# Performance work log

Hardware: AMD Instinct MI355X
Metric: run time of the kernel (lower is better)

## Reference

```python
import jax, jax.numpy as jnp
import numpy as np

N_EMBD = 1024
HEAD_SIZE = 64
T = 8192
LN_EPS = 1e-5


def _layer_norm(x, gamma, beta):
    mu = jnp.mean(x, axis=-1, keepdims=True)
    var = jnp.mean(jnp.square(x - mu), axis=-1, keepdims=True)
    return (x - mu) * jax.lax.rsqrt(var + LN_EPS) * gamma + beta


def setup_inputs() -> dict:
    key = jax.random.key(0)
    ks = jax.random.split(key, 10)
    s_in = 1.0 / np.sqrt(N_EMBD)
    s_hs = 1.0 / np.sqrt(HEAD_SIZE)
    s_ff = 1.0 / np.sqrt(4 * N_EMBD)
    return {
        "x": jax.random.normal(ks[0], (T, N_EMBD), dtype=jnp.float32),
        "Wk": jax.random.uniform(ks[1], (N_EMBD, HEAD_SIZE), jnp.float32, -s_in, s_in),
        "Wq": jax.random.uniform(ks[2], (N_EMBD, HEAD_SIZE), jnp.float32, -s_in, s_in),
        "Wv": jax.random.uniform(ks[3], (N_EMBD, HEAD_SIZE), jnp.float32, -s_in, s_in),
        "Wp": jax.random.uniform(ks[4], (HEAD_SIZE, N_EMBD), jnp.float32, -s_hs, s_hs),
        "W1": jax.random.uniform(ks[5], (N_EMBD, 4 * N_EMBD), jnp.float32, -s_in, s_in),
        "b1": jax.random.uniform(ks[6], (4 * N_EMBD,), jnp.float32, -s_in, s_in),
        "W2": jax.random.uniform(ks[7], (4 * N_EMBD, N_EMBD), jnp.float32, -s_ff, s_ff),
        "b2": jax.random.uniform(ks[8], (N_EMBD,), jnp.float32, -s_ff, s_ff),
        "g1": jnp.ones((N_EMBD,), jnp.float32),
        "be1": jnp.zeros((N_EMBD,), jnp.float32),
        "g2": jnp.ones((N_EMBD,), jnp.float32),
        "be2": jnp.zeros((N_EMBD,), jnp.float32),
    }


def reference(x, Wk, Wq, Wv, Wp, W1, b1, W2, b2, g1, be1, g2, be2):
    Tn = x.shape[0]
    k = x @ Wk            # (T, hs)
    q = x @ Wq            # (T, hs)
    v = x @ Wv            # (T, hs)
    wei = (q @ k.T) * (HEAD_SIZE ** -0.5)       # (T, T)
    causal = jnp.tril(jnp.ones((Tn, Tn), dtype=bool))
    wei = jnp.where(causal, wei, -jnp.inf)
    wei = jax.nn.softmax(wei, axis=-1)
    attn = (wei @ v) @ Wp                        # (T, n_embd)
    x1 = _layer_norm(x + attn, g1, be1)
    y = jax.nn.relu(x1 @ W1 + b1) @ W2 + b2      # FFN
    return _layer_norm(x1 + y, g2, be2)
```

## Files before the change

kernel.cpp:

```cpp
#include <hip/hip_runtime.h>
#include <hip/hip_bf16.h>

#define T_SEQ 8192
#define NE 1024
#define FF 4096

typedef __bf16 bf16_t;
typedef __bf16 bf16x8 __attribute__((ext_vector_type(8)));
typedef __bf16 bf16x4 __attribute__((ext_vector_type(4)));
typedef float f32x4 __attribute__((ext_vector_type(4)));

__device__ __forceinline__ void gll16(const void* g, void* l) {
    __builtin_amdgcn_global_load_lds(
        (const __attribute__((address_space(1))) void*)g,
        (__attribute__((address_space(3))) void*)l, 16, 0, 0);
}

__global__ __launch_bounds__(256) void cast_f32_bf16(const float* __restrict__ in,
                                                     bf16_t* __restrict__ out, int n4) {
    int i = blockIdx.x * 256 + threadIdx.x;
    if (i >= n4) return;
    float4 v = ((const float4*)in)[i];
    bf16x4 h;
    h[0] = (bf16_t)v.x; h[1] = (bf16_t)v.y; h[2] = (bf16_t)v.z; h[3] = (bf16_t)v.w;
    ((bf16x4*)out)[i] = h;
}

__global__ __launch_bounds__(256) void build_wkqv(const float* __restrict__ Wk,
                                                  const float* __restrict__ Wq,
                                                  const float* __restrict__ Wv,
                                                  bf16_t* __restrict__ out) {
    int idx = blockIdx.x * 256 + threadIdx.x;
    int n  = idx >> 10;
    int kk = idx & 1023;
    float v = 0.f;
    if (n < 64)       v = Wk[kk * 64 + n];
    else if (n < 128) v = Wq[kk * 64 + (n - 64)] * 0.125f;
    else if (n < 192) v = Wv[kk * 64 + (n - 128)];
    out[idx] = (bf16_t)v;
}

__global__ __launch_bounds__(256) void tcast(const float* __restrict__ in,
                                             bf16_t* __restrict__ out, int R, int C) {
    __shared__ bf16_t tl[64][66];
    const int bc = blockIdx.x << 6, br = blockIdx.y << 6;
    const int tx = threadIdx.x & 63, ty = threadIdx.x >> 6;
#pragma unroll
    for (int j = 0; j < 16; ++j) {
        const int r = ty + j * 4;
        tl[r][tx] = (bf16_t)in[(size_t)(br + r) * C + bc + tx];
    }
    __syncthreads();
#pragma unroll
    for (int j = 0; j < 16; ++j) {
        const int r = ty + j * 4;
        out[(size_t)(bc + r) * R + br + tx] = tl[tx][r];
    }
}

template <int EPI>
__global__ __launch_bounds__(256, 2)
void gemm_bt(const bf16_t* __restrict__ A, const bf16_t* __restrict__ Bt,
             int M, int N, int K,
             float* __restrict__ outf,
             bf16_t* __restrict__ ob0, bf16_t* __restrict__ ob1, bf16_t* __restrict__ ob2,
             const float* __restrict__ res, const float* __restrict__ bias) {
    const int tid  = threadIdx.x;
    const int lane = tid & 63;
    const int tiles_n = N >> 7;
    const int tm = blockIdx.x / tiles_n;
    const int tn = blockIdx.x % tiles_n;
    const int brow = tm << 7, bcol = tn << 7;

    __shared__ __align__(16) bf16_t As[128 * 32];
    __shared__ __align__(16) bf16_t Bs[128 * 32];

    const int c1 = tid, c2 = tid + 256;
    const int s1 = (((c1 & 3) ^ ((c1 >> 3) & 3)) * 8);
    const int s2 = (((c2 & 3) ^ ((c2 >> 3) & 3)) * 8);
    const bf16_t* gA1 = A + (size_t)(brow + (c1 >> 2)) * K + s1;
    const bf16_t* gA2 = A + (size_t)(brow + (c2 >> 2)) * K + s2;
    const bf16_t* gB1 = Bt + (size_t)(bcol + (c1 >> 2)) * K + s1;
    const bf16_t* gB2 = Bt + (size_t)(bcol + (c2 >> 2)) * K + s2;
    bf16_t* lA1 = As + c1 * 8; bf16_t* lA2 = As + c2 * 8;
    bf16_t* lB1 = Bs + c1 * 8; bf16_t* lB2 = Bs + c2 * 8;

    const int wv = tid >> 6;
    const int wr = (wv >> 1) * 64, wc = (wv & 1) * 64;
    const int arow  = wr + (lane & 15);
    const int brf   = wc + (lane & 15);
    const int koff = (((lane >> 4) ^ ((lane >> 1) & 3)) * 8);

    f32x4 acc[4][4];
#pragma unroll
    for (int i = 0; i < 4; ++i)
#pragma unroll
        for (int j = 0; j < 4; ++j) acc[i][j] = (f32x4){0.f, 0.f, 0.f, 0.f};

    for (int k0 = 0; k0 < K; k0 += 32) {
        gll16(gA1, lA1); gll16(gA2, lA2);
        gll16(gB1, lB1); gll16(gB2, lB2);
        gA1 += 32; gA2 += 32; gB1 += 32; gB2 += 32;
        __syncthreads();
        bf16x8 af[4], bfr[4];
#pragma unroll
        for (int mi = 0; mi < 4; ++mi)
            af[mi] = *(const bf16x8*)(As + (arow + mi * 16) * 32 + koff);
#pragma unroll
        for (int ni = 0; ni < 4; ++ni)
            bfr[ni] = *(const bf16x8*)(Bs + (brf + ni * 16) * 32 + koff);
#pragma unroll
        for (int mi = 0; mi < 4; ++mi)
#pragma unroll
            for (int ni = 0; ni < 4; ++ni)
                acc[mi][ni] = __builtin_amdgcn_mfma_f32_16x16x32_bf16(
                    af[mi], bfr[ni], acc[mi][ni], 0, 0, 0);
        __syncthreads();
    }

    const int r0 = brow + wr + ((lane >> 4) << 2);
    const int c0 = bcol + wc + (lane & 15);
#pragma unroll
    for (int mi = 0; mi < 4; ++mi)
#pragma unroll
        for (int ni = 0; ni < 4; ++ni)
#pragma unroll
            for (int r = 0; r < 4; ++r) {
                const int row = r0 + mi * 16 + r;
                const int col = c0 + ni * 16;
                const float v = acc[mi][ni][r];
                if constexpr (EPI == 0) {
                    if (col < 64)       ob0[row * 64 + col] = (bf16_t)v;
                    else if (col < 128) ob1[row * 64 + (col - 64)] = (bf16_t)v;
                    else if (col < 192) ob2[(size_t)(col - 128) * T_SEQ + row] = (bf16_t)v;
                } else if constexpr (EPI == 1) {
                    outf[(size_t)row * N + col] = res[(size_t)row * N + col] + v;
                } else if constexpr (EPI == 2) {
                    ob0[(size_t)row * N + col] = (bf16_t)fmaxf(v + bias[col], 0.f);
                } else {
                    outf[(size_t)row * N + col] = res[(size_t)row * N + col] + v + bias[col];
                }
            }
}

template <int EPI>
__global__ __launch_bounds__(512, 1)
void gemm_ls(const bf16_t* __restrict__ A, int lda,
             const bf16_t* __restrict__ Bt, int ldb,
             int N, int K,
             bf16_t* __restrict__ ob, const float* __restrict__ bias,
             float* __restrict__ po0, float* __restrict__ po1) {
    __shared__ __align__(16) bf16_t sA[4][8192];
    __shared__ __align__(16) bf16_t sB[4][8192];
    const int tid = threadIdx.x, lane = tid & 63, w = tid >> 6;
    const int wm = w >> 2, wn = w & 3;
    const int nwg = gridDim.x;
    const int wgid = (blockIdx.x & 7) * (nwg >> 3) + (blockIdx.x >> 3);
    const int tiles_n = N >> 8;
    const int tm = wgid / tiles_n, tn = wgid % tiles_n;
    const int brow = tm << 8, bcol = tn << 8;
    const size_t kofs = (size_t)blockIdx.y * K;
    const int s0 = (w & 1) * 2, rbb = w >> 1;
    const bf16_t* gA0 = A + (size_t)(brow + rbb * 64 + lane) * lda + kofs + s0 * 8;
    const bf16_t* gB0 = Bt + (size_t)(bcol + rbb * 64 + lane) * ldb + kofs + s0 * 8;
    const int dA0 = s0 * 2048 + (rbb * 64 + lane) * 8;
    const int l15 = lane & 15, sq = lane >> 4;
    const int aoff = sq * 2048 + (wm * 128 + l15) * 8;
    const int boff = sq * 2048 + (wn * 64 + l15) * 8;
    const int NTS = K >> 5;
    f32x4 acc[8][4];
#pragma unroll
    for (int i = 0; i < 8; ++i)
#pragma unroll
        for (int j = 0; j < 4; ++j) acc[i][j] = (f32x4){0.f, 0.f, 0.f, 0.f};
    bf16x8 af[8], bfr[4];
#define L_SB  __builtin_amdgcn_sched_barrier(0)
#define L_BAR { L_SB; __builtin_amdgcn_s_barrier(); L_SB; }
#define L_LG0 { asm volatile("s_waitcnt lgkmcnt(0)" ::: "memory"); L_SB; }
#define L_VM4 { asm volatile("s_waitcnt vmcnt(4)" ::: "memory"); L_SB; }
#define L_VM0 { asm volatile("s_waitcnt vmcnt(0)" ::: "memory"); L_SB; }
#define L_STAGE(t) { const int q_ = (t) & 3; \
    gll16(gA0 + (size_t)(t) * 32,        &sA[q_][dA0]); \
    gll16(gA0 + (size_t)(t) * 32 + 8,    &sA[q_][dA0 + 2048]); \
    gll16(gB0 + (size_t)(t) * 32,        &sB[q_][dA0]); \
    gll16(gB0 + (size_t)(t) * 32 + 8,    &sB[q_][dA0 + 2048]); \
    L_SB; }
#define L_DS(t) { const int q_ = (t) & 3; \
    _Pragma("unroll") for (int m = 0; m < 8; ++m) \
        af[m] = *(const bf16x8*)(&sA[q_][aoff + m * 128]); \
    _Pragma("unroll") for (int n = 0; n < 4; ++n) \
        bfr[n] = *(const bf16x8*)(&sB[q_][boff + n * 128]); }
#define L_MMA() { __builtin_amdgcn_s_setprio(1); \
    _Pragma("unroll") for (int m = 0; m < 8; ++m) \
    _Pragma("unroll") for (int n = 0; n < 4; ++n) \
        acc[m][n] = __builtin_amdgcn_mfma_f32_16x16x32_bf16(af[m], bfr[n], acc[m][n], 0, 0, 0); \
    __builtin_amdgcn_s_setprio(0); }
    L_STAGE(0); L_STAGE(1);
    L_VM4; L_BAR;
    for (int t = 0; t < NTS - 2; ++t) {
        L_DS(t);
        L_STAGE(t + 2);
        L_LG0;
        L_MMA();
        L_VM4; L_BAR;
    }
    L_DS(NTS - 2); L_LG0; L_MMA(); L_VM0; L_BAR;
    L_DS(NTS - 1); L_LG0; L_MMA();
#undef L_MMA
#undef L_DS
#undef L_STAGE
#undef L_VM0
#undef L_VM4
#undef L_LG0
#undef L_BAR
#undef L_SB
    const int r0 = brow + wm * 128 + sq * 4;
    const int c0 = bcol + wn * 64 + l15;
    float* po = blockIdx.y ? po1 : po0;
#pragma unroll
    for (int m = 0; m < 8; ++m)
#pragma unroll
        for (int n = 0; n < 4; ++n) {
            const int col = c0 + n * 16;
#pragma unroll
            for (int r = 0; r < 4; ++r) {
                const int row = r0 + m * 16 + r;
                const float v = acc[m][n][r];
                if constexpr (EPI == 2) {
                    ob[(size_t)row * N + col] = (bf16_t)fmaxf(v + bias[col], 0.f);
                } else {
                    po[(size_t)row * N + col] = v;
                }
            }
        }
}

template <int EPI>
__global__ __launch_bounds__(512, 2)
void gemm_bn128(const bf16_t* __restrict__ A, int lda,
                const bf16_t* __restrict__ Bt, int ldb,
                int N, int K,
                bf16_t* __restrict__ ob, const float* __restrict__ bias,
                float* __restrict__ po0, float* __restrict__ po1) {
    __shared__ __align__(16) bf16_t sA[3][8192];
    __shared__ __align__(16) bf16_t sB[3][4096];
    const int tid = threadIdx.x, lane = tid & 63, w = tid >> 6;
    const int wm = w >> 1, wn = w & 1;

    const int nwg = gridDim.x;
    const int wgid = (blockIdx.x & 7) * (nwg >> 3) + (blockIdx.x >> 3);
    const int tiles_n = N >> 7;
    const int tm = wgid / tiles_n, tn = wgid % tiles_n;
    const int brow = tm << 8, bcol = tn << 7;
    const size_t kofs = (size_t)blockIdx.y * K;

    const int cA0 = w * 2, cA1 = w * 2 + 1;
    const bf16_t* gA_0 = A + (size_t)(brow + (cA0 >> 2) * 64 + lane) * lda + kofs + (cA0 & 3) * 8;
    const bf16_t* gA_1 = A + (size_t)(brow + (cA1 >> 2) * 64 + lane) * lda + kofs + (cA1 & 3) * 8;
    const int dA_0 = (cA0 & 3) * 2048 + ((cA0 >> 2) * 64 + lane) * 8;
    const int dA_1 = (cA1 & 3) * 2048 + ((cA1 >> 2) * 64 + lane) * 8;
    const bf16_t* gB_0 = Bt + (size_t)(bcol + (w >> 2) * 64 + lane) * ldb + kofs + (w & 3) * 8;
    const int dB_0 = (w & 3) * 1024 + ((w >> 2) * 64 + lane) * 8;

    const int l15 = lane & 15, sq = lane >> 4;
    const int aoff = sq * 2048 + (wm * 64 + l15) * 8;
    const int boff = sq * 1024 + (wn * 64 + l15) * 8;
    const int NTS = K >> 5;

    f32x4 acc[4][4];
#pragma unroll
    for (int i = 0; i < 4; ++i)
#pragma unroll
        for (int j = 0; j < 4; ++j) acc[i][j] = (f32x4){0.f, 0.f, 0.f, 0.f};
    bf16x8 af[4], bfr[4];

#define N_SB  __builtin_amdgcn_sched_barrier(0)
#define N_BAR { N_SB; __builtin_amdgcn_s_barrier(); N_SB; }
#define N_LG0 { asm volatile("s_waitcnt lgkmcnt(0)" ::: "memory"); N_SB; }
#define N_VM3 { asm volatile("s_waitcnt vmcnt(3)" ::: "memory"); N_SB; }
#define N_VM0 { asm volatile("s_waitcnt vmcnt(0)" ::: "memory"); N_SB; }
#define N_STAGE(t) { const int q_ = (t) % 3; \
    gll16(gA_0 + (size_t)(t) * 32, &sA[q_][dA_0]); \
    gll16(gA_1 + (size_t)(t) * 32, &sA[q_][dA_1]); \
    gll16(gB_0 + (size_t)(t) * 32, &sB[q_][dB_0]); \
    N_SB; }
#define N_DS(t) { const int q_ = (t) % 3; \
    _Pragma("unroll") for (int m = 0; m < 4; ++m) \
        af[m] = *(const bf16x8*)(&sA[q_][aoff + m * 128]); \
    _Pragma("unroll") for (int n = 0; n < 4; ++n) \
        bfr[n] = *(const bf16x8*)(&sB[q_][boff + n * 128]); }
#define N_MMA() { __builtin_amdgcn_s_setprio(1); \
    _Pragma("unroll") for (int m = 0; m < 4; ++m) \
    _Pragma("unroll") for (int n = 0; n < 4; ++n) \
        acc[m][n] = __builtin_amdgcn_mfma_f32_16x16x32_bf16(af[m], bfr[n], acc[m][n], 0, 0, 0); \
    __builtin_amdgcn_s_setprio(0); }

    N_STAGE(0); N_STAGE(1);
    N_VM3; N_BAR;
    for (int t = 0; t < NTS - 2; ++t) {
        N_DS(t);
        N_STAGE(t + 2);
        N_LG0;
        N_MMA();
        N_VM3; N_BAR;
    }
    N_DS(NTS - 2); N_LG0; N_MMA(); N_VM0; N_BAR;
    N_DS(NTS - 1); N_LG0; N_MMA();

#undef N_MMA
#undef N_DS
#undef N_STAGE
#undef N_VM0
#undef N_VM3
#undef N_LG0
#undef N_BAR
#undef N_SB

    const int r0 = brow + wm * 64 + (sq << 2);
    const int c0 = bcol + wn * 64 + l15;
    float* po = blockIdx.y ? po1 : po0;
#pragma unroll
    for (int m = 0; m < 4; ++m)
#pragma unroll
        for (int n = 0; n < 4; ++n) {
            const int col = c0 + n * 16;
#pragma unroll
            for (int r = 0; r < 4; ++r) {
                const int row = r0 + m * 16 + r;
                const float v = acc[m][n][r];
                if constexpr (EPI == 2) {
                    ob[(size_t)row * N + col] = (bf16_t)fmaxf(v + bias[col], 0.f);
                } else {
                    po[(size_t)row * N + col] = v;
                }
            }
        }
}

__global__ __launch_bounds__(256)
void attn_partial(const bf16_t* __restrict__ Q, const bf16_t* __restrict__ Kb,
                  const bf16_t* __restrict__ VT,
                  float* __restrict__ po, float* __restrict__ pml) {
    const int tid = threadIdx.x, lane = tid & 63, w = tid >> 6;
    const int j = blockIdx.x * 4 + w;

    int a = 0;
    while (j >= 16 * (a + 1) * (a + 2)) ++a;
    const int r_in = j - 16 * a * (a + 1);
    const int idx = r_in / (a + 1);
    const int chunk = r_in - idx * (a + 1);
    const int g = a * 8 + (idx >> 2);
    const int qi = g * 4 + (idx & 3);
    const int G = g >> 1;

    __shared__ __align__(16) bf16_t P[4][16 * 128];
    const int l15 = lane & 15, hi = lane >> 4;
    const int koff = hi * 8;
    const int qrow = qi * 16 + l15;
    const bf16x8 qf0 = *(const bf16x8*)(Q + qrow * 64 + koff);
    const bf16x8 qf1 = *(const bf16x8*)(Q + qrow * 64 + 32 + koff);

    float m_run[4], l_run[4];
    f32x4 oacc[4];
#pragma unroll
    for (int r = 0; r < 4; ++r) { m_run[r] = -1e30f; l_run[r] = 0.f; }
#pragma unroll
    for (int d = 0; d < 4; ++d) oacc[d] = (f32x4){0.f, 0.f, 0.f, 0.f};

    const int t0 = chunk * 4;
    const int t1 = min(t0 + 4, G + 1);
    for (int t = t0; t < t1; ++t) {
        const int kv0 = t << 7;
        f32x4 s[8];
#pragma unroll
        for (int ni = 0; ni < 8; ++ni) s[ni] = (f32x4){0.f, 0.f, 0.f, 0.f};
#pragma unroll
        for (int ni = 0; ni < 8; ++ni) {
            const bf16_t* kp = Kb + (size_t)(kv0 + ni * 16 + l15) * 64 + koff;
            bf16x8 kf0 = *(const bf16x8*)(kp);
            bf16x8 kf1 = *(const bf16x8*)(kp + 32);
            s[ni] = __builtin_amdgcn_mfma_f32_16x16x32_bf16(qf0, kf0, s[ni], 0, 0, 0);
            s[ni] = __builtin_amdgcn_mfma_f32_16x16x32_bf16(qf1, kf1, s[ni], 0, 0, 0);
        }
        if (t == G) {
#pragma unroll
            for (int ni = 0; ni < 8; ++ni)
#pragma unroll
                for (int r = 0; r < 4; ++r) {
                    const int col = kv0 + ni * 16 + l15;
                    const int row = qi * 16 + hi * 4 + r;
                    if (col > row) s[ni][r] = -1e30f;
                }
        }
        float alpha[4];
#pragma unroll
        for (int r = 0; r < 4; ++r) {
            float vm = fmaxf(fmaxf(fmaxf(s[0][r], s[1][r]), fmaxf(s[2][r], s[3][r])),
                             fmaxf(fmaxf(s[4][r], s[5][r]), fmaxf(s[6][r], s[7][r])));
            vm = fmaxf(vm, __shfl_xor(vm, 1));
            vm = fmaxf(vm, __shfl_xor(vm, 2));
            vm = fmaxf(vm, __shfl_xor(vm, 4));
            vm = fmaxf(vm, __shfl_xor(vm, 8));
            const float mnew = fmaxf(m_run[r], vm);
            float sum = 0.f;
#pragma unroll
            for (int ni = 0; ni < 8; ++ni) {
                const float p = __expf(s[ni][r] - mnew);
                s[ni][r] = p;
                sum += p;
            }
            sum += __shfl_xor(sum, 1); sum += __shfl_xor(sum, 2);
            sum += __shfl_xor(sum, 4); sum += __shfl_xor(sum, 8);
            alpha[r] = __expf(m_run[r] - mnew);
            l_run[r] = l_run[r] * alpha[r] + sum;
            m_run[r] = mnew;
        }
#pragma unroll
        for (int d = 0; d < 4; ++d)
#pragma unroll
            for (int r = 0; r < 4; ++r) oacc[d][r] *= alpha[r];
        bf16x8 vcur[4], vnxt[4];
#pragma unroll
        for (int d = 0; d < 4; ++d)
            vcur[d] = *(const bf16x8*)(VT + (size_t)(d * 16 + l15) * T_SEQ + kv0 + koff);
        asm volatile("s_waitcnt lgkmcnt(0)" ::: "memory");
        __builtin_amdgcn_sched_barrier(0);
#pragma unroll
        for (int ni = 0; ni < 8; ++ni)
#pragma unroll
            for (int r = 0; r < 4; ++r)
                P[w][(hi * 4 + r) * 128 + ni * 16 + l15] = (bf16_t)s[ni][r];
        asm volatile("s_waitcnt lgkmcnt(0)" ::: "memory");
        __builtin_amdgcn_sched_barrier(0);
#pragma unroll
        for (int ks = 0; ks < 4; ++ks) {
            bf16x8 pf = *(const bf16x8*)(&P[w][l15 * 128 + ks * 32 + koff]);
            if (ks < 3) {
#pragma unroll
                for (int d = 0; d < 4; ++d)
                    vnxt[d] = *(const bf16x8*)(VT + (size_t)(d * 16 + l15) * T_SEQ +
                                               kv0 + (ks + 1) * 32 + koff);
            }
#pragma unroll
            for (int d = 0; d < 4; ++d)
                oacc[d] = __builtin_amdgcn_mfma_f32_16x16x32_bf16(pf, vcur[d], oacc[d], 0, 0, 0);
#pragma unroll
            for (int d = 0; d < 4; ++d) vcur[d] = vnxt[d];
        }
    }
#pragma unroll
    for (int d = 0; d < 4; ++d)
#pragma unroll
        for (int r = 0; r < 4; ++r)
            po[(size_t)j * 1024 + (hi * 4 + r) * 64 + d * 16 + l15] = oacc[d][r];
    if (l15 == 0) {
#pragma unroll
        for (int r = 0; r < 4; ++r) {
            pml[(size_t)j * 32 + hi * 4 + r] = m_run[r];
            pml[(size_t)j * 32 + 16 + hi * 4 + r] = l_run[r];
        }
    }
}

__global__ __launch_bounds__(256)
void attn_reduce(const float* __restrict__ po, const float* __restrict__ pml,
                 bf16_t* __restrict__ O) {
    const int qi = blockIdx.x;
    const int tid = threadIdx.x;
    const int row = tid >> 4;
    const int cg = tid & 15;
    const int g = qi >> 2;
    const int a = g >> 3;
    const int idx = ((g & 7) << 2) | (qi & 3);
    const int base = 16 * a * (a + 1) + idx * (a + 1);
    const int cnt = a + 1;

    float M = -1e30f;
    for (int i = 0; i < cnt; ++i)
        M = fmaxf(M, pml[(size_t)(base + i) * 32 + row]);
    float L = 0.f;
    f32x4 o = (f32x4){0.f, 0.f, 0.f, 0.f};
    for (int i = 0; i < cnt; ++i) {
        const float m = pml[(size_t)(base + i) * 32 + row];
        const float l = pml[(size_t)(base + i) * 32 + 16 + row];
        const float wgt = __expf(m - M);
        L += l * wgt;
        const f32x4 v = *(const f32x4*)&po[(size_t)(base + i) * 1024 + row * 64 + cg * 4];
#pragma unroll
        for (int u = 0; u < 4; ++u) o[u] += v[u] * wgt;
    }
    const float inv = 1.f / L;
    bf16x4 h;
#pragma unroll
    for (int u = 0; u < 4; ++u) h[u] = (bf16_t)(o[u] * inv);
    *(bf16x4*)(O + (size_t)(qi * 16 + row) * 64 + cg * 4) = h;
}

__global__ __launch_bounds__(256)
void ln_fused(const float* __restrict__ in, const float* __restrict__ g,
              const float* __restrict__ b, float* __restrict__ o32,
              bf16_t* __restrict__ o16) {
    const int row = blockIdx.x, tid = threadIdx.x;
    const float4 v = ((const float4*)(in + (size_t)row * NE))[tid];
    float s = v.x + v.y + v.z + v.w;
    float ss = v.x * v.x + v.y * v.y + v.z * v.z + v.w * v.w;
#pragma unroll
    for (int off = 1; off < 64; off <<= 1) {
        s  += __shfl_xor(s, off);
        ss += __shfl_xor(ss, off);
    }
    __shared__ float red[8];
    const int wv = tid >> 6, lane = tid & 63;
    if (lane == 0) { red[wv] = s; red[4 + wv] = ss; }
    __syncthreads();
    s  = red[0] + red[1] + red[2] + red[3];
    ss = red[4] + red[5] + red[6] + red[7];
    const float mu = s * (1.f / NE);
    const float rstd = rsqrtf(ss * (1.f / NE) - mu * mu + 1e-5f);
    const float4 gg = ((const float4*)g)[tid];
    const float4 bb = ((const float4*)b)[tid];
    float4 o;
    o.x = (v.x - mu) * rstd * gg.x + bb.x;
    o.y = (v.y - mu) * rstd * gg.y + bb.y;
    o.z = (v.z - mu) * rstd * gg.z + bb.z;
    o.w = (v.w - mu) * rstd * gg.w + bb.w;
    if (o32) ((float4*)(o32 + (size_t)row * NE))[tid] = o;
    if (o16) {
        bf16x4 h;
        h[0] = (bf16_t)o.x; h[1] = (bf16_t)o.y; h[2] = (bf16_t)o.z; h[3] = (bf16_t)o.w;
        *(bf16x4*)(o16 + (size_t)row * NE + tid * 4) = h;
    }
}

__global__ __launch_bounds__(256)
void ln_sum(const float* __restrict__ r1, const float* __restrict__ p0,
            const float* __restrict__ p1, const float* __restrict__ bias,
            const float* __restrict__ g, const float* __restrict__ b,
            float* __restrict__ out) {
    const int row = blockIdx.x, tid = threadIdx.x;
    const size_t off = (size_t)row * NE;
    const float4 a = ((const float4*)(r1 + off))[tid];
    const float4 q0 = ((const float4*)(p0 + off))[tid];
    const float4 q1 = ((const float4*)(p1 + off))[tid];
    const float4 bb4 = ((const float4*)bias)[tid];
    float4 v;
    v.x = a.x + q0.x + q1.x + bb4.x;
    v.y = a.y + q0.y + q1.y + bb4.y;
    v.z = a.z + q0.z + q1.z + bb4.z;
    v.w = a.w + q0.w + q1.w + bb4.w;
    float s = v.x + v.y + v.z + v.w;
    float ss = v.x * v.x + v.y * v.y + v.z * v.z + v.w * v.w;
#pragma unroll
    for (int off2 = 1; off2 < 64; off2 <<= 1) {
        s  += __shfl_xor(s, off2);
        ss += __shfl_xor(ss, off2);
    }
    __shared__ float red[8];
    const int wv = tid >> 6, lane = tid & 63;
    if (lane == 0) { red[wv] = s; red[4 + wv] = ss; }
    __syncthreads();
    s  = red[0] + red[1] + red[2] + red[3];
    ss = red[4] + red[5] + red[6] + red[7];
    const float mu = s * (1.f / NE);
    const float rstd = rsqrtf(ss * (1.f / NE) - mu * mu + 1e-5f);
    const float4 gg = ((const float4*)g)[tid];
    const float4 be = ((const float4*)b)[tid];
    float4 o;
    o.x = (v.x - mu) * rstd * gg.x + be.x;
    o.y = (v.y - mu) * rstd * gg.y + be.y;
    o.z = (v.z - mu) * rstd * gg.z + be.z;
    o.w = (v.w - mu) * rstd * gg.w + be.w;
    ((float4*)(out + off))[tid] = o;
}

extern "C" void kernel_launch(void* const* d_in, const int* in_sizes, int n_in,
                              void* d_out, int out_size, void* d_ws, size_t ws_size,
                              hipStream_t stream) {
    (void)in_sizes; (void)n_in; (void)out_size; (void)ws_size;
    const float* x   = (const float*)d_in[0];
    const float* Wk  = (const float*)d_in[1];
    const float* Wq  = (const float*)d_in[2];
    const float* Wv  = (const float*)d_in[3];
    const float* Wp  = (const float*)d_in[4];
    const float* W1  = (const float*)d_in[5];
    const float* b1  = (const float*)d_in[6];
    const float* W2  = (const float*)d_in[7];
    const float* b2  = (const float*)d_in[8];
    const float* g1  = (const float*)d_in[9];
    const float* be1 = (const float*)d_in[10];
    const float* g2  = (const float*)d_in[11];
    const float* be2 = (const float*)d_in[12];
    float* out = (float*)d_out;

    char* ws = (char*)d_ws;
    bf16_t* xb   = (bf16_t*)(ws);
    bf16_t* x1b  = (bf16_t*)(ws + 16777216);
    bf16_t* hb   = (bf16_t*)(ws + 33554432);
    float*  po   = (float*)(ws + 33554432);
    float*  pml  = (float*)(ws + 33554432 + 18874368);
    bf16_t* W1t  = (bf16_t*)(ws + 100663296);
    bf16_t* W2t  = (bf16_t*)(ws + 109051904);
    bf16_t* Wkqv = (bf16_t*)(ws + 117440512);
    bf16_t* WpT  = (bf16_t*)(ws + 117964800);
    bf16_t* kb   = (bf16_t*)(ws + 118095872);
    bf16_t* qb   = (bf16_t*)(ws + 119144448);
    bf16_t* vT   = (bf16_t*)(ws + 120193024);
    bf16_t* a0   = (bf16_t*)(ws + 121241600);
    float*  r1   = (float*)(ws + 122290176);
    float*  pk0  = (float*)(ws + 155844608);
    float*  pk1  = (float*)(ws);

    cast_f32_bf16<<<8192, 256, 0, stream>>>(x, xb, 2097152);
    build_wkqv<<<1024, 256, 0, stream>>>(Wk, Wq, Wv, Wkqv);
    tcast<<<dim3(16, 1), 256, 0, stream>>>(Wp, WpT, 64, 1024);
    tcast<<<dim3(64, 16), 256, 0, stream>>>(W1, W1t, 1024, 4096);
    tcast<<<dim3(16, 64), 256, 0, stream>>>(W2, W2t, 4096, 1024);

    gemm_bt<0><<<64 * 2, 256, 0, stream>>>(xb, Wkqv, 8192, 256, 1024,
                                           nullptr, kb, qb, vT, nullptr, nullptr);
    attn_partial<<<1088, 256, 0, stream>>>(qb, kb, vT, po, pml);
    attn_reduce<<<512, 256, 0, stream>>>(po, pml, a0);
    gemm_bt<1><<<64 * 8, 256, 0, stream>>>(a0, WpT, 8192, 1024, 64,
                                           r1, nullptr, nullptr, nullptr, x, nullptr);
    ln_fused<<<8192, 256, 0, stream>>>(r1, g1, be1, r1, x1b);
    gemm_bn128<2><<<dim3(1024, 1), 512, 0, stream>>>(x1b, 1024, W1t, 1024, 4096, 1024,
                                                     hb, b1, nullptr, nullptr);
    gemm_ls<4><<<dim3(128, 2), 512, 0, stream>>>(hb, 4096, W2t, 4096, 1024, 2048,
                                                 nullptr, nullptr, pk0, pk1);
    ln_sum<<<8192, 256, 0, stream>>>(r1, pk0, pk1, b2, g2, be2, out);
}
```

Baseline: 389.9 us.

## Replace FFN1 GEMM 256x128 triple-buffered tile with 256x256 double-buffered tile

The first FFN GEMM moves from a 256x128 block tile with a 3-stage LDS ring to a 256x256 tile with 2-stage buffering. Each wave now computes 128x64 instead of 64x64, which raises arithmetic intensity and halves the number of workgroups. The load schedule waits on vmcnt(0) every step, so there is less prefetch depth. Launch bounds ask for 4 waves/SIMD occupancy even though accumulator registers double, which risks spills.

```diff
diff --git a/kernel.cpp b/kernel.cpp
--- a/kernel.cpp
+++ b/kernel.cpp
@@ -236,91 +236,78 @@
 }
 
 template <int EPI>
-__global__ __launch_bounds__(512, 2)
-void gemm_bn128(const bf16_t* __restrict__ A, int lda,
-                const bf16_t* __restrict__ Bt, int ldb,
-                int N, int K,
-                bf16_t* __restrict__ ob, const float* __restrict__ bias,
-                float* __restrict__ po0, float* __restrict__ po1) {
-    __shared__ __align__(16) bf16_t sA[3][8192];
-    __shared__ __align__(16) bf16_t sB[3][4096];
+__global__ __launch_bounds__(512, 4)
+void gemm_ls2(const bf16_t* __restrict__ A, int lda,
+              const bf16_t* __restrict__ Bt, int ldb,
+              int N, int K,
+              bf16_t* __restrict__ ob, const float* __restrict__ bias,
+              float* __restrict__ po0, float* __restrict__ po1) {
+    __shared__ __align__(16) bf16_t sA[2][8192];
+    __shared__ __align__(16) bf16_t sB[2][8192];
     const int tid = threadIdx.x, lane = tid & 63, w = tid >> 6;
-    const int wm = w >> 1, wn = w & 1;
-
+    const int wm = w >> 2, wn = w & 3;
     const int nwg = gridDim.x;
     const int wgid = (blockIdx.x & 7) * (nwg >> 3) + (blockIdx.x >> 3);
-    const int tiles_n = N >> 7;
+    const int tiles_n = N >> 8;
     const int tm = wgid / tiles_n, tn = wgid % tiles_n;
-    const int brow = tm << 8, bcol = tn << 7;
+    const int brow = tm << 8, bcol = tn << 8;
     const size_t kofs = (size_t)blockIdx.y * K;
-
-    const int cA0 = w * 2, cA1 = w * 2 + 1;
-    const bf16_t* gA_0 = A + (size_t)(brow + (cA0 >> 2) * 64 + lane) * lda + kofs + (cA0 & 3) * 8;
-    const bf16_t* gA_1 = A + (size_t)(brow + (cA1 >> 2) * 64 + lane) * lda + kofs + (cA1 & 3) * 8;
-    const int dA_0 = (cA0 & 3) * 2048 + ((cA0 >> 2) * 64 + lane) * 8;
-    const int dA_1 = (cA1 & 3) * 2048 + ((cA1 >> 2) * 64 + lane) * 8;
-    const bf16_t* gB_0 = Bt + (size_t)(bcol + (w >> 2) * 64 + lane) * ldb + kofs + (w & 3) * 8;
-    const int dB_0 = (w & 3) * 1024 + ((w >> 2) * 64 + lane) * 8;
-
+    const int s0 = (w & 1) * 2, rbb = w >> 1;
+    const bf16_t* gA0 = A + (size_t)(brow + rbb * 64 + lane) * lda + kofs + s0 * 8;
+    const bf16_t* gB0 = Bt + (size_t)(bcol + rbb * 64 + lane) * ldb + kofs + s0 * 8;
+    const int dA0 = s0 * 2048 + (rbb * 64 + lane) * 8;
     const int l15 = lane & 15, sq = lane >> 4;
-    const int aoff = sq * 2048 + (wm * 64 + l15) * 8;
-    const int boff = sq * 1024 + (wn * 64 + l15) * 8;
+    const int aoff = sq * 2048 + (wm * 128 + l15) * 8;
+    const int boff = sq * 2048 + (wn * 64 + l15) * 8;
     const int NTS = K >> 5;
-
-    f32x4 acc[4][4];
-#pragma unroll
-    for (int i = 0; i < 4; ++i)
+    f32x4 acc[8][4];
+#pragma unroll
+    for (int i = 0; i < 8; ++i)
 #pragma unroll
         for (int j = 0; j < 4; ++j) acc[i][j] = (f32x4){0.f, 0.f, 0.f, 0.f};
-    bf16x8 af[4], bfr[4];
-
-#define N_SB  __builtin_amdgcn_sched_barrier(0)
-#define N_BAR { N_SB; __builtin_amdgcn_s_barrier(); N_SB; }
-#define N_LG0 { asm volatile("s_waitcnt lgkmcnt(0)" ::: "memory"); N_SB; }
-#define N_VM3 { asm volatile("s_waitcnt vmcnt(3)" ::: "memory"); N_SB; }
-#define N_VM0 { asm volatile("s_waitcnt vmcnt(0)" ::: "memory"); N_SB; }
-#define N_STAGE(t) { const int q_ = (t) % 3; \
-    gll16(gA_0 + (size_t)(t) * 32, &sA[q_][dA_0]); \
-    gll16(gA_1 + (size_t)(t) * 32, &sA[q_][dA_1]); \
-    gll16(gB_0 + (size_t)(t) * 32, &sB[q_][dB_0]); \
-    N_SB; }
-#define N_DS(t) { const int q_ = (t) % 3; \
-    _Pragma("unroll") for (int m = 0; m < 4; ++m) \
+    bf16x8 af[8], bfr[4];
+#define D_SB  __builtin_amdgcn_sched_barrier(0)
+#define D_BAR { D_SB; __builtin_amdgcn_s_barrier(); D_SB; }
+#define D_LG0 { asm volatile("s_waitcnt lgkmcnt(0)" ::: "memory"); D_SB; }
+#define D_VM0 { asm volatile("s_waitcnt vmcnt(0)" ::: "memory"); D_SB; }
+#define D_STAGE(t) { const int q_ = (t) & 1; \
+    gll16(gA0 + (size_t)(t) * 32,        &sA[q_][dA0]); \
+    gll16(gA0 + (size_t)(t) * 32 + 8,    &sA[q_][dA0 + 2048]); \
+    gll16(gB0 + (size_t)(t) * 32,        &sB[q_][dA0]); \
+    gll16(gB0 + (size_t)(t) * 32 + 8,    &sB[q_][dA0 + 2048]); \
+    D_SB; }
+#define D_DS(t) { const int q_ = (t) & 1; \
+    _Pragma("unroll") for (int m = 0; m < 8; ++m) \
         af[m] = *(const bf16x8*)(&sA[q_][aoff + m * 128]); \
     _Pragma("unroll") for (int n = 0; n < 4; ++n) \
         bfr[n] = *(const bf16x8*)(&sB[q_][boff + n * 128]); }
-#define N_MMA() { __builtin_amdgcn_s_setprio(1); \
-    _Pragma("unroll") for (int m = 0; m < 4; ++m) \
+#define D_MMA() { __builtin_amdgcn_s_setprio(1); \
+    _Pragma("unroll") for (int m = 0; m < 8; ++m) \
     _Pragma("unroll") for (int n = 0; n < 4; ++n) \
         acc[m][n] = __builtin_amdgcn_mfma_f32_16x16x32_bf16(af[m], bfr[n], acc[m][n], 0, 0, 0); \
     __builtin_amdgcn_s_setprio(0); }
-
-    N_STAGE(0); N_STAGE(1);
-    N_VM3; N_BAR;
-    for (int t = 0; t < NTS - 2; ++t) {
-        N_DS(t);
-        N_STAGE(t + 2);
-        N_LG0;
-        N_MMA();
-        N_VM3; N_BAR;
-    }
-    N_DS(NTS - 2); N_LG0; N_MMA(); N_VM0; N_BAR;
-    N_DS(NTS - 1); N_LG0; N_MMA();
-
-#undef N_MMA
-#undef N_DS
-#undef N_STAGE
-#undef N_VM0
-#undef N_VM3
-#undef N_LG0
-#undef N_BAR
-#undef N_SB
-
-    const int r0 = brow + wm * 64 + (sq << 2);
+    D_STAGE(0);
+    D_VM0; D_BAR;
+    for (int t = 0; t < NTS - 1; ++t) {
+        D_DS(t);
+        D_STAGE(t + 1);
+        D_LG0;
+        D_MMA();
+        D_VM0; D_BAR;
+    }
+    D_DS(NTS - 1); D_LG0; D_MMA();
+#undef D_MMA
+#undef D_DS
+#undef D_STAGE
+#undef D_VM0
+#undef D_LG0
+#undef D_BAR
+#undef D_SB
+    const int r0 = brow + wm * 128 + sq * 4;
     const int c0 = bcol + wn * 64 + l15;
     float* po = blockIdx.y ? po1 : po0;
 #pragma unroll
-    for (int m = 0; m < 4; ++m)
+    for (int m = 0; m < 8; ++m)
 #pragma unroll
         for (int n = 0; n < 4; ++n) {
             const int col = c0 + n * 16;
@@ -623,8 +610,8 @@
     gemm_bt<1><<<64 * 8, 256, 0, stream>>>(a0, WpT, 8192, 1024, 64,
                                            r1, nullptr, nullptr, nullptr, x, nullptr);
     ln_fused<<<8192, 256, 0, stream>>>(r1, g1, be1, r1, x1b);
-    gemm_bn128<2><<<dim3(1024, 1), 512, 0, stream>>>(x1b, 1024, W1t, 1024, 4096, 1024,
-                                                     hb, b1, nullptr, nullptr);
+    gemm_ls2<2><<<dim3(512, 1), 512, 0, stream>>>(x1b, 1024, W1t, 1024, 4096, 1024,
+                                                  hb, b1, nullptr, nullptr);
     gemm_ls<4><<<dim3(128, 2), 512, 0, stream>>>(hb, 4096, W2t, 4096, 1024, 2048,
                                                  nullptr, nullptr, pk0, pk1);
     ln_sum<<<8192, 256, 0, stream>>>(r1, pk0, pk1, b2, g2, be2, out);
```

Result: slower. 1.033 ms (+165.0%).
